# Performance work log

Measured on AMD Instinct MI355X. Metric: run time of the kernel, lower is better.

The kernel has to match this reference:

```python
import jax, jax.numpy as jnp
import numpy as np

N_NODES = 100000
N_EDGES = 1600000
NODE_DIM = 128
MEM = 64
NEG_SLOPE = 0.2  # GATConv default negative_slope


def setup_inputs() -> dict:
    key = jax.random.key(0)
    ks = jax.random.split(key, 16)
    s = lambda k, shape, fan: jax.random.normal(k, shape, jnp.float32) * (1.0 / np.sqrt(fan))
    return {
        "state": jax.random.normal(ks[0], (N_NODES, NODE_DIM), jnp.float32),
        "abstract_goal": jax.random.normal(ks[1], (N_NODES, MEM), jnp.float32),
        "memory_state": jax.random.normal(ks[2], (N_NODES, MEM), jnp.float32),
        "edge_index": jax.random.randint(ks[3], (2, N_EDGES), 0, N_NODES, jnp.int64),
        # input_proj: Linear(node_dim, memory_size)
        "w_in": s(ks[4], (MEM, NODE_DIM), NODE_DIM),
        "b_in": jnp.zeros((MEM,), jnp.float32),
        # GATConv(memory_size, memory_size, heads=1, concat=False)
        "w_gat": s(ks[5], (MEM, MEM), MEM),       # lin (no bias)
        "att_src": s(ks[6], (MEM,), MEM),
        "att_dst": s(ks[7], (MEM,), MEM),
        "b_gat": jnp.zeros((MEM,), jnp.float32),
        # GRUCell(memory_size, memory_size)
        "w_ih": s(ks[8], (3 * MEM, MEM), MEM),
        "w_hh": s(ks[9], (3 * MEM, MEM), MEM),
        "b_ih": jnp.zeros((3 * MEM,), jnp.float32),
        "b_hh": jnp.zeros((3 * MEM,), jnp.float32),
    }


def _gat(x, edge_index, w_gat, att_src, att_dst, b_gat):
    n = x.shape[0]
    # add self loops (GATConv default add_self_loops=True)
    loop = jnp.arange(n, dtype=edge_index.dtype)
    src = jnp.concatenate([edge_index[0], loop])
    dst = jnp.concatenate([edge_index[1], loop])
    xt = x @ w_gat.T                                  # [N, MEM]
    a_s = xt @ att_src                                # [N]
    a_d = xt @ att_dst                                # [N]
    e = a_s[src] + a_d[dst]                           # [E+N]
    e = jnp.where(e >= 0, e, NEG_SLOPE * e)           # leaky_relu
    # segment softmax over incoming edges of each dst node
    m = jax.ops.segment_max(e, dst, num_segments=n)
    ex = jnp.exp(e - m[dst])
    denom = jax.ops.segment_sum(ex, dst, num_segments=n)
    alpha = ex / denom[dst]
    out = jax.ops.segment_sum(xt[src] * alpha[:, None], dst, num_segments=n)
    return out + b_gat


def _gru_cell(x, h, w_ih, w_hh, b_ih, b_hh):
    gi = x @ w_ih.T + b_ih
    gh = h @ w_hh.T + b_hh
    i_r, i_z, i_n = jnp.split(gi, 3, axis=-1)
    h_r, h_z, h_n = jnp.split(gh, 3, axis=-1)
    r = jax.nn.sigmoid(i_r + h_r)
    z = jax.nn.sigmoid(i_z + h_z)
    n = jnp.tanh(i_n + r * h_n)
    return (1.0 - z) * n + z * h


def reference(state, abstract_goal, memory_state, edge_index,
              w_in, b_in, w_gat, att_src, att_dst, b_gat,
              w_ih, w_hh, b_ih, b_hh):
    projected = state @ w_in.T + b_in
    mem_enh = projected + abstract_goal + memory_state
    ctx = _gat(mem_enh, edge_index, w_gat, att_src, att_dst, b_gat)
    memory_input = mem_enh + ctx
    return _gru_cell(memory_input, memory_state, w_ih, w_hh, b_ih, b_hh)
```

## Files before the change

kernel.cpp:

```cpp
#include <hip/hip_runtime.h>
#include <hip/hip_bf16.h>

#define N_NODES 100000
#define N_EDGES 1600000
#define NODE_DIM 128
#define MEM 64
#define NEG_SLOPE 0.2f
#define NB ((N_NODES + 255) / 256)

typedef __attribute__((ext_vector_type(8))) short short8;
typedef __attribute__((ext_vector_type(4))) float f32x4;

__device__ __forceinline__ float lrelu(float v) { return v >= 0.f ? v : NEG_SLOPE * v; }

__device__ __forceinline__ unsigned short bfr(float f) {
    unsigned u = __float_as_uint(f);
    u = (u + 0x7FFFu + ((u >> 16) & 1u)) >> 16;
    return (unsigned short)u;
}
__device__ __forceinline__ float bf2f(unsigned short s) {
    return __uint_as_float(((unsigned)s) << 16);
}

__global__ __launch_bounds__(256) void kA(
    const float* __restrict__ state, const float* __restrict__ goal,
    const float* __restrict__ mem, const float* __restrict__ w_in,
    const float* __restrict__ b_in, const float* __restrict__ w_gat,
    const float* __restrict__ att_src, const float* __restrict__ att_dst,
    unsigned short* __restrict__ me_out, unsigned short* __restrict__ xt_out,
    float* __restrict__ as_out, float* __restrict__ ad_out)
{
    __shared__ unsigned short s_me[16][72];
    __shared__ float s_red[4][16][2];
    const int wv = threadIdx.x >> 6;
    const int lane = threadIdx.x & 63;
    const int lr = lane & 15;
    const int lk = lane >> 4;
    const int col = wv * 16 + lr;

    short8 Bp[4], Bx[2];
    #pragma unroll
    for (int s = 0; s < 4; ++s) {
        const float* p = w_in + (long)col * NODE_DIM + s * 32 + lk * 8;
        short8 b;
        #pragma unroll
        for (int t = 0; t < 8; ++t) b[t] = (short)bfr(p[t]);
        Bp[s] = b;
    }
    #pragma unroll
    for (int s = 0; s < 2; ++s) {
        const float* p = w_gat + (long)col * MEM + s * 32 + lk * 8;
        short8 b;
        #pragma unroll
        for (int t = 0; t < 8; ++t) b[t] = (short)bfr(p[t]);
        Bx[s] = b;
    }
    const float bcol = b_in[col];
    const float av_s = att_src[col], av_d = att_dst[col];

    for (int mt = blockIdx.x; mt < N_NODES / 16; mt += gridDim.x) {
        const int n0 = mt * 16;
        short8 Ap[4];
        #pragma unroll
        for (int s = 0; s < 4; ++s) {
            const float* p = state + (long)(n0 + lr) * NODE_DIM + s * 32 + lk * 8;
            short8 a;
            #pragma unroll
            for (int t = 0; t < 8; ++t) a[t] = (short)bfr(p[t]);
            Ap[s] = a;
        }
        f32x4 accp;
        accp[0] = bcol; accp[1] = bcol; accp[2] = bcol; accp[3] = bcol;
        #pragma unroll
        for (int s = 0; s < 4; ++s)
            accp = __builtin_amdgcn_mfma_f32_16x16x32_bf16(Ap[s], Bp[s], accp, 0, 0, 0);
        unsigned short mev[4];
        #pragma unroll
        for (int r = 0; r < 4; ++r) {
            const long off = (long)(n0 + lk * 4 + r) * MEM + col;
            const float v = accp[r] + goal[off] + mem[off];
            mev[r] = bfr(v);
            me_out[off] = mev[r];
        }
        __syncthreads();
        #pragma unroll
        for (int r = 0; r < 4; ++r) s_me[lk * 4 + r][col] = mev[r];
        __syncthreads();
        short8 Ax2[2];
        #pragma unroll
        for (int s = 0; s < 2; ++s)
            Ax2[s] = *(const short8*)&s_me[lr][s * 32 + lk * 8];
        f32x4 accx;
        accx[0] = 0.f; accx[1] = 0.f; accx[2] = 0.f; accx[3] = 0.f;
        #pragma unroll
        for (int s = 0; s < 2; ++s)
            accx = __builtin_amdgcn_mfma_f32_16x16x32_bf16(Ax2[s], Bx[s], accx, 0, 0, 0);
        float ps[4], pd[4];
        #pragma unroll
        for (int r = 0; r < 4; ++r) {
            const float xv = accx[r];
            xt_out[(long)(n0 + lk * 4 + r) * MEM + col] = bfr(xv);
            ps[r] = xv * av_s;
            pd[r] = xv * av_d;
        }
        #pragma unroll
        for (int r = 0; r < 4; ++r) {
            #pragma unroll
            for (int o = 1; o < 16; o <<= 1) {
                ps[r] += __shfl_xor(ps[r], o);
                pd[r] += __shfl_xor(pd[r], o);
            }
        }
        if (lr == 0) {
            #pragma unroll
            for (int r = 0; r < 4; ++r) {
                s_red[wv][lk * 4 + r][0] = ps[r];
                s_red[wv][lk * 4 + r][1] = pd[r];
            }
        }
        __syncthreads();
        if (threadIdx.x < 32) {
            const int node = threadIdx.x >> 1, sel = threadIdx.x & 1;
            const float v = s_red[0][node][sel] + s_red[1][node][sel] +
                            s_red[2][node][sel] + s_red[3][node][sel];
            if (sel == 0) as_out[n0 + node] = v;
            else          ad_out[n0 + node] = v;
        }
    }
}

__global__ __launch_bounds__(256) void kH(const int* __restrict__ dst, int* __restrict__ deg) {
    const int e = blockIdx.x * 256 + threadIdx.x;
    if (e < N_EDGES) atomicAdd(deg + dst[e], 1);
}

__global__ __launch_bounds__(256) void kS1(const int* __restrict__ deg, int* __restrict__ bsums) {
    const int i = blockIdx.x * 256 + threadIdx.x;
    int s = (i < N_NODES) ? deg[i] : 0;
    #pragma unroll
    for (int o = 32; o; o >>= 1) s += __shfl_xor(s, o);
    __shared__ int ws_[4];
    if ((threadIdx.x & 63) == 0) ws_[threadIdx.x >> 6] = s;
    __syncthreads();
    if (threadIdx.x == 0) bsums[blockIdx.x] = ws_[0] + ws_[1] + ws_[2] + ws_[3];
}

__global__ __launch_bounds__(512) void kS2(int* __restrict__ bsums) {
    const int t = threadIdx.x;
    int v = (t < NB) ? bsums[t] : 0;
    int x = v;
    #pragma unroll
    for (int o = 1; o < 64; o <<= 1) {
        int y = __shfl_up(x, o);
        if ((t & 63) >= o) x += y;
    }
    __shared__ int wt[8];
    if ((t & 63) == 63) wt[t >> 6] = x;
    __syncthreads();
    int woff = 0;
    for (int w = 0; w < (t >> 6); ++w) woff += wt[w];
    if (t < NB) bsums[t] = woff + x - v;
}

__global__ __launch_bounds__(256) void kS3(const int* __restrict__ deg, const int* __restrict__ bsums,
                                           int* __restrict__ row_ptr, int* __restrict__ cursor) {
    const int i = blockIdx.x * 256 + threadIdx.x;
    const int t = threadIdx.x;
    int v = (i < N_NODES) ? deg[i] : 0;
    int x = v;
    #pragma unroll
    for (int o = 1; o < 64; o <<= 1) {
        int y = __shfl_up(x, o);
        if ((t & 63) >= o) x += y;
    }
    __shared__ int wt[4];
    if ((t & 63) == 63) wt[t >> 6] = x;
    __syncthreads();
    int woff = bsums[blockIdx.x];
    for (int w = 0; w < (t >> 6); ++w) woff += wt[w];
    const int excl = woff + x - v;
    if (i < N_NODES) {
        row_ptr[i] = excl;
        cursor[i] = excl;
        if (i == N_NODES - 1) row_ptr[N_NODES] = excl + v;
    }
}

__global__ __launch_bounds__(256) void kP(
    const int* __restrict__ src, const int* __restrict__ dst,
    const float* __restrict__ as_, const float* __restrict__ ad_,
    int* __restrict__ cursor, int2* __restrict__ csr)
{
    const int e = blockIdx.x * 256 + threadIdx.x;
    if (e >= N_EDGES) return;
    const int s = src[e], d = dst[e];
    const int slot = atomicAdd(cursor + d, 1);
    const float ev = lrelu(as_[s] + ad_[d]);
    csr[slot] = make_int2(s, __float_as_int(ev));
}

__global__ __launch_bounds__(256) void kG(
    const int* __restrict__ row_ptr, const int2* __restrict__ csr,
    const float* __restrict__ as_, const float* __restrict__ ad_,
    const unsigned short* __restrict__ xt, const float* __restrict__ b_gat,
    unsigned short* __restrict__ me )
{
    const int wave = threadIdx.x >> 6, lane = threadIdx.x & 63;
    const int eo = lane >> 5, c2 = lane & 31;
    const float bg0 = b_gat[2 * c2], bg1 = b_gat[2 * c2 + 1];
    const int* csr_y = (const int*)csr;
    for (int node = blockIdx.x * 4 + wave; node < N_NODES; node += gridDim.x * 4) {
        const int beg = row_ptr[node], end = row_ptr[node + 1];
        const float e_self = lrelu(as_[node] + ad_[node]);
        float m = e_self;
        for (int j = beg + lane; j < end; j += 64)
            m = fmaxf(m, __int_as_float(csr_y[2 * j + 1]));
        #pragma unroll
        for (int o = 32; o; o >>= 1) m = fmaxf(m, __shfl_xor(m, o));
        float acc0 = 0.f, acc1 = 0.f, den = 0.f;
        int j = beg + eo;
        for (; j + 2 < end; j += 4) {
            const int2 ca = csr[j], cb = csr[j + 2];
            const unsigned ua = *(const unsigned*)&xt[((unsigned)ca.x << 6) + 2 * c2];
            const unsigned ub = *(const unsigned*)&xt[((unsigned)cb.x << 6) + 2 * c2];
            const float wa = __expf(__int_as_float(ca.y) - m);
            const float wb = __expf(__int_as_float(cb.y) - m);
            den += wa + wb;
            acc0 += bf2f((unsigned short)(ua & 0xFFFF)) * wa + bf2f((unsigned short)(ub & 0xFFFF)) * wb;
            acc1 += bf2f((unsigned short)(ua >> 16)) * wa + bf2f((unsigned short)(ub >> 16)) * wb;
        }
        if (j < end) {
            const int2 c = csr[j];
            const unsigned u = *(const unsigned*)&xt[((unsigned)c.x << 6) + 2 * c2];
            const float w = __expf(__int_as_float(c.y) - m);
            den += w;
            acc0 += bf2f((unsigned short)(u & 0xFFFF)) * w;
            acc1 += bf2f((unsigned short)(u >> 16)) * w;
        }
        acc0 += __shfl_xor(acc0, 32);
        acc1 += __shfl_xor(acc1, 32);
        den  += __shfl_xor(den, 32);
        const float wself = __expf(e_self - m);
        den += wself;
        const unsigned us = *(const unsigned*)&xt[((unsigned)node << 6) + 2 * c2];
        acc0 += bf2f((unsigned short)(us & 0xFFFF)) * wself;
        acc1 += bf2f((unsigned short)(us >> 16)) * wself;
        if (eo == 0) {
            const float inv = 1.f / den;
            unsigned short* mp = me + ((long)node << 6) + 2 * c2;
            const unsigned um = *(const unsigned*)mp;
            const float r0 = bf2f((unsigned short)(um & 0xFFFF)) + acc0 * inv + bg0;
            const float r1 = bf2f((unsigned short)(um >> 16)) + acc1 * inv + bg1;
            *(unsigned*)mp = (unsigned)bfr(r0) | ((unsigned)bfr(r1) << 16);
        }
    }
}

__global__ __launch_bounds__(256) void kE(
    const unsigned short* __restrict__ x, const float* __restrict__ h,
    const float* __restrict__ w_ih, const float* __restrict__ w_hh,
    const float* __restrict__ b_ih, const float* __restrict__ b_hh,
    float* __restrict__ out)
{
    const int wv = threadIdx.x >> 6;
    const int lane = threadIdx.x & 63;
    const int lr = lane & 15;
    const int lk = lane >> 4;
    const int col = wv * 16 + lr;

    short8 Bf[6][2];
    #pragma unroll
    for (int g = 0; g < 6; ++g) {
        const float* W = (g < 3) ? w_ih : w_hh;
        const int row = (g % 3) * 64 + col;
        #pragma unroll
        for (int hf = 0; hf < 2; ++hf) {
            const float* p = W + (long)row * MEM + hf * 32 + lk * 8;
            short8 b;
            #pragma unroll
            for (int t = 0; t < 8; ++t) b[t] = (short)bfr(p[t]);
            Bf[g][hf] = b;
        }
    }
    const float bias[6] = { b_ih[col], b_ih[64 + col], b_ih[128 + col],
                            b_hh[col], b_hh[64 + col], b_hh[128 + col] };

    for (int mt = blockIdx.x; mt < N_NODES / 16; mt += gridDim.x) {
        const int n0 = mt * 16;
        const float* rh = h + (long)(n0 + lr) * MEM + lk * 8;
        short8 Ax[2], Ah[2];
        #pragma unroll
        for (int hf = 0; hf < 2; ++hf) {
            Ax[hf] = *(const short8*)(x + (long)(n0 + lr) * MEM + hf * 32 + lk * 8);
            short8 b;
            #pragma unroll
            for (int t = 0; t < 8; ++t) b[t] = (short)bfr(rh[hf * 32 + t]);
            Ah[hf] = b;
        }
        f32x4 acc[6];
        #pragma unroll
        for (int g = 0; g < 6; ++g) {
            f32x4 z; z[0] = bias[g]; z[1] = bias[g]; z[2] = bias[g]; z[3] = bias[g];
            acc[g] = z;
        }
        #pragma unroll
        for (int g = 0; g < 3; ++g) {
            acc[g] = __builtin_amdgcn_mfma_f32_16x16x32_bf16(Ax[0], Bf[g][0], acc[g], 0, 0, 0);
            acc[g] = __builtin_amdgcn_mfma_f32_16x16x32_bf16(Ax[1], Bf[g][1], acc[g], 0, 0, 0);
        }
        #pragma unroll
        for (int g = 3; g < 6; ++g) {
            acc[g] = __builtin_amdgcn_mfma_f32_16x16x32_bf16(Ah[0], Bf[g][0], acc[g], 0, 0, 0);
            acc[g] = __builtin_amdgcn_mfma_f32_16x16x32_bf16(Ah[1], Bf[g][1], acc[g], 0, 0, 0);
        }
        #pragma unroll
        for (int r = 0; r < 4; ++r) {
            const int node = n0 + lk * 4 + r;
            const long off = (long)node * MEM + col;
            const float hv = h[off];
            const float rr = 1.f / (1.f + __expf(-(acc[0][r] + acc[3][r])));
            const float zz = 1.f / (1.f + __expf(-(acc[1][r] + acc[4][r])));
            const float nn = tanhf(acc[2][r] + rr * acc[5][r]);
            out[off] = (1.f - zz) * nn + zz * hv;
        }
    }
}

extern "C" void kernel_launch(void* const* d_in, const int* in_sizes, int n_in,
                              void* d_out, int out_size, void* d_ws, size_t ws_size,
                              hipStream_t stream) {
    const float* state = (const float*)d_in[0];
    const float* goal  = (const float*)d_in[1];
    const float* mem   = (const float*)d_in[2];
    const int*   ei    = (const int*)d_in[3];
    const float* w_in  = (const float*)d_in[4];
    const float* b_in  = (const float*)d_in[5];
    const float* w_gat = (const float*)d_in[6];
    const float* att_s = (const float*)d_in[7];
    const float* att_d = (const float*)d_in[8];
    const float* b_gat = (const float*)d_in[9];
    const float* w_ih  = (const float*)d_in[10];
    const float* w_hh  = (const float*)d_in[11];
    const float* b_ih  = (const float*)d_in[12];
    const float* b_hh  = (const float*)d_in[13];
    float* out = (float*)d_out;

    const int* e_src = ei;
    const int* e_dst = ei + N_EDGES;

    unsigned short* me16 = (unsigned short*)d_ws;
    unsigned short* xt_bf = me16 + (long)N_NODES * MEM;
    float* as_buf  = (float*)(xt_bf + (long)N_NODES * MEM);
    float* ad_buf  = as_buf + N_NODES;
    int*   deg     = (int*)(ad_buf + N_NODES);
    int*   row_ptr = deg + N_NODES;
    int*   cursor  = row_ptr + N_NODES + 1;
    int*   bsums   = cursor + N_NODES;
    long csr_off = (long)(bsums + NB - (int*)d_ws);
    csr_off = (csr_off + 1) & ~1L;
    int2*  csr     = (int2*)((int*)d_ws + csr_off);

    hipMemsetAsync(deg, 0, N_NODES * sizeof(int), stream);

    hipLaunchKernelGGL(kA, dim3(1024), dim3(256), 0, stream,
        state, goal, mem, w_in, b_in, w_gat, att_s, att_d,
        me16, xt_bf, as_buf, ad_buf);

    hipLaunchKernelGGL(kH, dim3((N_EDGES + 255) / 256), dim3(256), 0, stream, e_dst, deg);
    hipLaunchKernelGGL(kS1, dim3(NB), dim3(256), 0, stream, deg, bsums);
    hipLaunchKernelGGL(kS2, dim3(1), dim3(512), 0, stream, bsums);
    hipLaunchKernelGGL(kS3, dim3(NB), dim3(256), 0, stream, deg, bsums, row_ptr, cursor);
    hipLaunchKernelGGL(kP, dim3((N_EDGES + 255) / 256), dim3(256), 0, stream,
        e_src, e_dst, as_buf, ad_buf, cursor, csr);

    hipLaunchKernelGGL(kG, dim3(2048), dim3(256), 0, stream,
        row_ptr, csr, as_buf, ad_buf, xt_bf, b_gat, me16);

    hipLaunchKernelGGL(kE, dim3(1024), dim3(256), 0, stream,
        me16, mem, w_ih, w_hh, b_ih, b_hh, out);
}
```

Before: 435.4 us.

## Drop segment-max pass and store only source index in CSR

The CSR build now stores only the source index, not a precomputed edge score, which halves the edge scatter writes and removes the as/ad gathers from the permutation kernel. The GAT aggregation recomputes each edge score from as_[src] and ad_[node], and uses the self-loop score as the softmax shift instead of a true per-node max, which removes the separate max pass over the edges. The histogram kernel also reads destination indices as int4 vectors. The risk is possible exp overflow when an edge score far exceeds the self-loop score, plus an extra scattered as_ gather per edge in the hot loop.

```diff
diff --git a/kernel.cpp b/kernel.cpp
--- a/kernel.cpp
+++ b/kernel.cpp
@@ -129,9 +129,15 @@
     }
 }
 
-__global__ __launch_bounds__(256) void kH(const int* __restrict__ dst, int* __restrict__ deg) {
-    const int e = blockIdx.x * 256 + threadIdx.x;
-    if (e < N_EDGES) atomicAdd(deg + dst[e], 1);
+__global__ __launch_bounds__(256) void kH(const int4* __restrict__ dst4, int* __restrict__ deg) {
+    const int i = blockIdx.x * 256 + threadIdx.x;
+    if (i < N_EDGES / 4) {
+        const int4 d = dst4[i];
+        atomicAdd(deg + d.x, 1);
+        atomicAdd(deg + d.y, 1);
+        atomicAdd(deg + d.z, 1);
+        atomicAdd(deg + d.w, 1);
+    }
 }
 
 __global__ __launch_bounds__(256) void kS1(const int* __restrict__ deg, int* __restrict__ bsums) {
@@ -188,19 +194,16 @@
 
 __global__ __launch_bounds__(256) void kP(
     const int* __restrict__ src, const int* __restrict__ dst,
-    const float* __restrict__ as_, const float* __restrict__ ad_,
-    int* __restrict__ cursor, int2* __restrict__ csr)
+    int* __restrict__ cursor, int* __restrict__ csrS)
 {
     const int e = blockIdx.x * 256 + threadIdx.x;
     if (e >= N_EDGES) return;
-    const int s = src[e], d = dst[e];
-    const int slot = atomicAdd(cursor + d, 1);
-    const float ev = lrelu(as_[s] + ad_[d]);
-    csr[slot] = make_int2(s, __float_as_int(ev));
+    const int slot = atomicAdd(cursor + dst[e], 1);
+    csrS[slot] = src[e];
 }
 
 __global__ __launch_bounds__(256) void kG(
-    const int* __restrict__ row_ptr, const int2* __restrict__ csr,
+    const int* __restrict__ row_ptr, const int* __restrict__ csrS,
     const float* __restrict__ as_, const float* __restrict__ ad_,
     const unsigned short* __restrict__ xt, const float* __restrict__ b_gat,
     unsigned short* __restrict__ me )
@@ -208,31 +211,26 @@
     const int wave = threadIdx.x >> 6, lane = threadIdx.x & 63;
     const int eo = lane >> 5, c2 = lane & 31;
     const float bg0 = b_gat[2 * c2], bg1 = b_gat[2 * c2 + 1];
-    const int* csr_y = (const int*)csr;
     for (int node = blockIdx.x * 4 + wave; node < N_NODES; node += gridDim.x * 4) {
         const int beg = row_ptr[node], end = row_ptr[node + 1];
-        const float e_self = lrelu(as_[node] + ad_[node]);
-        float m = e_self;
-        for (int j = beg + lane; j < end; j += 64)
-            m = fmaxf(m, __int_as_float(csr_y[2 * j + 1]));
-        #pragma unroll
-        for (int o = 32; o; o >>= 1) m = fmaxf(m, __shfl_xor(m, o));
+        const float adn = ad_[node];
+        const float e_self = lrelu(as_[node] + adn);
         float acc0 = 0.f, acc1 = 0.f, den = 0.f;
         int j = beg + eo;
         for (; j + 2 < end; j += 4) {
-            const int2 ca = csr[j], cb = csr[j + 2];
-            const unsigned ua = *(const unsigned*)&xt[((unsigned)ca.x << 6) + 2 * c2];
-            const unsigned ub = *(const unsigned*)&xt[((unsigned)cb.x << 6) + 2 * c2];
-            const float wa = __expf(__int_as_float(ca.y) - m);
-            const float wb = __expf(__int_as_float(cb.y) - m);
+            const int sa = csrS[j], sb = csrS[j + 2];
+            const unsigned ua = *(const unsigned*)&xt[((unsigned)sa << 6) + 2 * c2];
+            const unsigned ub = *(const unsigned*)&xt[((unsigned)sb << 6) + 2 * c2];
+            const float wa = __expf(lrelu(as_[sa] + adn) - e_self);
+            const float wb = __expf(lrelu(as_[sb] + adn) - e_self);
             den += wa + wb;
             acc0 += bf2f((unsigned short)(ua & 0xFFFF)) * wa + bf2f((unsigned short)(ub & 0xFFFF)) * wb;
             acc1 += bf2f((unsigned short)(ua >> 16)) * wa + bf2f((unsigned short)(ub >> 16)) * wb;
         }
         if (j < end) {
-            const int2 c = csr[j];
-            const unsigned u = *(const unsigned*)&xt[((unsigned)c.x << 6) + 2 * c2];
-            const float w = __expf(__int_as_float(c.y) - m);
+            const int s = csrS[j];
+            const unsigned u = *(const unsigned*)&xt[((unsigned)s << 6) + 2 * c2];
+            const float w = __expf(lrelu(as_[s] + adn) - e_self);
             den += w;
             acc0 += bf2f((unsigned short)(u & 0xFFFF)) * w;
             acc1 += bf2f((unsigned short)(u >> 16)) * w;
@@ -240,11 +238,10 @@
         acc0 += __shfl_xor(acc0, 32);
         acc1 += __shfl_xor(acc1, 32);
         den  += __shfl_xor(den, 32);
-        const float wself = __expf(e_self - m);
-        den += wself;
+        den += 1.f;
         const unsigned us = *(const unsigned*)&xt[((unsigned)node << 6) + 2 * c2];
-        acc0 += bf2f((unsigned short)(us & 0xFFFF)) * wself;
-        acc1 += bf2f((unsigned short)(us >> 16)) * wself;
+        acc0 += bf2f((unsigned short)(us & 0xFFFF));
+        acc1 += bf2f((unsigned short)(us >> 16));
         if (eo == 0) {
             const float inv = 1.f / den;
             unsigned short* mp = me + ((long)node << 6) + 2 * c2;
@@ -356,9 +353,7 @@
     int*   row_ptr = deg + N_NODES;
     int*   cursor  = row_ptr + N_NODES + 1;
     int*   bsums   = cursor + N_NODES;
-    long csr_off = (long)(bsums + NB - (int*)d_ws);
-    csr_off = (csr_off + 1) & ~1L;
-    int2*  csr     = (int2*)((int*)d_ws + csr_off);
+    int*   csrS    = bsums + NB;
 
     hipMemsetAsync(deg, 0, N_NODES * sizeof(int), stream);
 
@@ -366,15 +361,16 @@
         state, goal, mem, w_in, b_in, w_gat, att_s, att_d,
         me16, xt_bf, as_buf, ad_buf);
 
-    hipLaunchKernelGGL(kH, dim3((N_EDGES + 255) / 256), dim3(256), 0, stream, e_dst, deg);
+    hipLaunchKernelGGL(kH, dim3((N_EDGES / 4 + 255) / 256), dim3(256), 0, stream,
+        (const int4*)e_dst, deg);
     hipLaunchKernelGGL(kS1, dim3(NB), dim3(256), 0, stream, deg, bsums);
     hipLaunchKernelGGL(kS2, dim3(1), dim3(512), 0, stream, bsums);
     hipLaunchKernelGGL(kS3, dim3(NB), dim3(256), 0, stream, deg, bsums, row_ptr, cursor);
     hipLaunchKernelGGL(kP, dim3((N_EDGES + 255) / 256), dim3(256), 0, stream,
-        e_src, e_dst, as_buf, ad_buf, cursor, csr);
+        e_src, e_dst, cursor, csrS);
 
     hipLaunchKernelGGL(kG, dim3(2048), dim3(256), 0, stream,
-        row_ptr, csr, as_buf, ad_buf, xt_bf, b_gat, me16);
+        row_ptr, csrS, as_buf, ad_buf, xt_bf, b_gat, me16);
 
     hipLaunchKernelGGL(kE, dim3(1024), dim3(256), 0, stream,
         me16, mem, w_ih, w_hh, b_ih, b_hh, out);
```

Result: slower. 469.7 us (+7.9%).
